# Performance work log

Measured on AMD Instinct MI355X. Metric: run time of the kernel, lower is better.

Reference implementation:

```python
import jax, jax.numpy as jnp
import numpy as np
from jax import lax

H = 256       # hidden_size (hard-coded via .view(256,1) in source)
V = 10000     # vocab
NOPS = 9      # ops: 0 sum, 1 count, 2 diff, 3 greater, 4 lesser, 5 and, 6 or, 7 assign, 8 reset
COLS = 64
ROWS = 200000
T = 4         # num_time_steps
QLEN = 40
NNUM = 5


def setup_inputs() -> dict:
    key = jax.random.key(0)
    ks = jax.random.split(key, 16)
    s = 0.02
    return {
        'input_question': jax.random.randint(ks[0], (QLEN,), 0, V),
        'question_numbers': jax.random.normal(ks[1], (NNUM,), jnp.float32),
        'left_word_indices': jax.random.randint(ks[2], (NNUM,), 0, QLEN),
        'table': jax.random.normal(ks[3], (ROWS, COLS), jnp.float32),
        # question RNN params
        'E': jax.random.normal(ks[4], (V, H), jnp.float32) * s,
        'Wx': jax.random.normal(ks[5], (H, H), jnp.float32) * s,
        'Wh': jax.random.normal(ks[6], (H, H), jnp.float32) * s,
        'b': jnp.zeros((H,), jnp.float32),
        # selector params
        'W_op': jax.random.normal(ks[7], (H, 2 * H), jnp.float32) * s,
        'op_emb': jax.random.normal(ks[8], (NOPS, H), jnp.float32) * s,
        'W_col': jax.random.normal(ks[9], (H, 2 * H), jnp.float32) * s,
        'col_emb': jax.random.normal(ks[10], (COLS, H), jnp.float32) * s,
        # pivot embeddings U(0)=lesser, U(1)=greater
        'U': jax.random.normal(ks[11], (2, H), jnp.float32) * s,
        # history RNN params
        'W_hc': jax.random.normal(ks[12], (H, 2 * H), jnp.float32) * s,
        'W_hh': jax.random.normal(ks[13], (H, H), jnp.float32) * s,
    }


def reference(input_question, question_numbers, left_word_indices, table,
              E, Wx, Wh, b, W_op, op_emb, W_col, col_emb, U, W_hc, W_hh):
    rows = table.shape[0]
    # ---- question RNN (simple tanh RNN over embedded words) ----
    x = E[input_question]                                  # [Q, H]
    def cell(h, xt):
        hn = jnp.tanh(xt @ Wx + h @ Wh + b)
        return hn, hn
    q, states = lax.scan(cell, jnp.zeros((H,), table.dtype), x)   # q: [H], states: [Q, H]
    Z = states[left_word_indices]                          # z_matrix [N, H]

    # ---- pivots (train mode: soft attention over question numbers) ----
    beta_l = jax.nn.softmax(Z @ U[0])                      # [N]
    beta_g = jax.nn.softmax(Z @ U[1])
    l_pivot = beta_l @ question_numbers                    # scalar
    g_pivot = beta_g @ question_numbers

    row_selects = [jnp.ones((rows,), table.dtype)]
    scalars = [jnp.zeros((), table.dtype)]
    h_hist = jnp.zeros((H,), table.dtype)
    lookup = jnp.zeros(table.shape, table.dtype)

    for t in range(T):
        qh = jnp.concatenate([q, h_hist])                  # [2H]
        a_op = jax.nn.softmax(op_emb @ jnp.tanh(W_op @ qh))    # [NOPS]
        a_col = jax.nn.softmax(col_emb @ jnp.tanh(W_col @ qh)) # [COLS]

        rs1 = row_selects[-1]
        rs2 = row_selects[max(0, len(row_selects) - 2)]
        s1 = scalars[-1]
        s3 = scalars[max(0, len(scalars) - 3)]

        col_val = table @ a_col                            # [R] column-weighted table values
        g_sel = (table > g_pivot).astype(table.dtype) @ a_col  # [R]
        l_sel = (table < l_pivot).astype(table.dtype) @ a_col

        row_select = (a_op[3] * g_sel + a_op[4] * l_sel
                      + a_op[5] * jnp.minimum(rs1, rs2)
                      + a_op[6] * jnp.maximum(rs1, rs2)
                      + a_op[8] * 1.0
                      + (a_op[0] + a_op[1] + a_op[2] + a_op[7]) * rs1)

        scalar = (a_op[0] * (rs1 @ col_val)
                  + a_op[1] * jnp.sum(rs1)
                  + a_op[2] * (s3 - s1))

        lookup = a_op[7] * row_select[:, None] * a_col[None, :]   # [R, C]

        c = jnp.concatenate([a_op @ op_emb, a_col @ col_emb])     # [2H]
        h_hist = jnp.tanh(W_hc @ c + W_hh @ h_hist)

        row_selects.append(row_select)
        scalars.append(scalar)

    return scalars[-1], lookup
```

## Files before the change

kernel.cpp:

```cpp
#include <hip/hip_runtime.h>
#include <math.h>

#define H 256
#define COLSN 64
#define ROWSN 200000
#define T_STEPS 4
#define QLEN 40
#define NNUM 5
#define NOPS 9

#define WS_UBUF   0
#define WS_XWB    0
#define WS_Q      10240
#define WS_AOP    10496
#define WS_ACOL   10560
#define WS_PIV    10816
#define WS_TICKET 10818
#define WS_PACC8  10824
#define WS_ARR    10832
#define WS_XWDONE 10836
#define WS_MDONE  10837
#define WS_QDONE  10838
#define WS_MOP    11104
#define WS_MCOL   13408

#define NTBL_TILES  1563
#define NTBL_BLOCKS 782
#define NW 12
#define NXW 10
#define NMB 72
#define NFUSED (NW + 1 + NXW + NMB)

template<int CTRL>
__device__ __forceinline__ float dpp_add(float x) {
    int xi = __float_as_int(x);
    int yi = __builtin_amdgcn_update_dpp(0, xi, CTRL, 0xF, 0xF, true);
    return x + __int_as_float(yi);
}
#define DPP_XOR1 0xB1
#define DPP_XOR2 0x4E
#define DPP_HMIR 0x141
#define DPP_MIR  0x140

__device__ __forceinline__ float reduce16(float v) {
    v = dpp_add<DPP_XOR1>(v);
    v = dpp_add<DPP_XOR2>(v);
    v = dpp_add<DPP_HMIR>(v);
    v = dpp_add<DPP_MIR>(v);
    return v;
}

__device__ __forceinline__ float fast_tanh(float x) {
    float cx = fminf(15.f, fmaxf(-15.f, x));
    float e = __expf(2.f * cx);
    return __fdividef(e - 1.f, e + 1.f);
}

__device__ __forceinline__ float dot4(float4 a, float4 b) {
    return a.x * b.x + a.y * b.y + a.z * b.z + a.w * b.w;
}

__device__ __forceinline__ float aread(float* p) { return atomicAdd(p, 0.f); }

__device__ __forceinline__ int sw(int i) { return i + ((i >> 4) << 2); }

__global__ void k_zero(float* __restrict__ ws) {
    int t = threadIdx.x;
    if (t < 22) ws[WS_TICKET + t] = 0.f;
}

__global__ __launch_bounds__(1024) void k_fused(
        const int* __restrict__ iq, const int* __restrict__ lwi,
        const float* __restrict__ qn, const float* __restrict__ E,
        const float* __restrict__ Wx, const float* __restrict__ b,
        const float* __restrict__ Wh, const float* __restrict__ U,
        const float* __restrict__ W_op, const float* __restrict__ W_col,
        const float* __restrict__ W_hh, const float* __restrict__ W_hc,
        const float* __restrict__ op_emb, const float* __restrict__ col_emb,
        float* __restrict__ ws) {
    __shared__ __attribute__((aligned(16))) float smem[36864];
    const int tid = threadIdx.x;
    const int blk = blockIdx.x;

    if (blk < NW) {
        float* wlds  = smem;
        float* mlds  = smem + 16448;
        float* hl    = smem + 35136;
        float* Pl    = smem + 35456;
        float* uop   = smem + 35520;
        float* ucol  = smem + 35840;
        float* vhh   = smem + 36160;
        float* lgs   = smem + 36416;
        float* aop_s = smem + 36496;
        float* acol_s= smem + 36512;
        const int wb = blk * 64;
        const int r  = tid >> 4;
        const int p  = tid & 15;
        const int pb = p * 20;

        for (int idx = tid; idx < 64 * 64; idx += 1024) {
            int rr = idx >> 6, j4 = idx & 63;
            int o = wb + rr;
            const float* src = (o < 256) ? &W_op[(long)o * 512 + 256]
                             : (o < 512) ? &W_col[(long)(o - 256) * 512 + 256]
                             : &W_hh[(long)(o - 512) * 256];
            float4 v = *(const float4*)&src[j4 * 4];
            float* d = &wlds[rr * 257 + j4 * 4];
            d[0] = v.x; d[1] = v.y; d[2] = v.z; d[3] = v.w;
        }
        if (tid == 0) while (aread(&ws[WS_MDONE]) < NMB - 0.5f) __builtin_amdgcn_s_sleep(8);
        __syncthreads();
        for (int idx = tid; idx < 73 * 256; idx += 1024)
            mlds[idx] = aread(&ws[WS_MOP + idx]);
        if (tid == 0) while (aread(&ws[WS_QDONE]) < 0.5f) __builtin_amdgcn_s_sleep(8);
        __syncthreads();
        if (tid < 256) hl[sw(tid)] = aread(&ws[WS_Q + tid]);
        __syncthreads();
        {
            int o = wb + r;
            float s = 0.f;
            if (o < 512) {
                const float* row = (o < 256) ? &W_op[(long)o * 512 + p * 16]
                                             : &W_col[(long)(o - 256) * 512 + p * 16];
                float4 r0 = *(const float4*)&row[0];
                float4 r1 = *(const float4*)&row[4];
                float4 r2 = *(const float4*)&row[8];
                float4 r3 = *(const float4*)&row[12];
                const float* qq = &hl[pb];
                s = dot4(r0, *(const float4*)&qq[0]) + dot4(r1, *(const float4*)&qq[4])
                  + dot4(r2, *(const float4*)&qq[8]) + dot4(r3, *(const float4*)&qq[12]);
            }
            s = reduce16(s);
            if (p == 0) Pl[r] = s;
        }
        __syncthreads();
        if (tid < 64) {
            int o = wb + tid;
            float val = (o < 512) ? fast_tanh(Pl[tid]) : 0.f;
            atomicExch(&ws[WS_UBUF + 0 * 768 + o], val);
        }
        __threadfence();
        __syncthreads();
        if (tid == 0) atomicAdd(&ws[WS_ARR + 0], 1.f);

        for (int t = 0; t < T_STEPS; ++t) {
            if (tid == 0) while (aread(&ws[WS_ARR + t]) < NW - 0.5f) __builtin_amdgcn_s_sleep(1);
            __syncthreads();
            if (tid < 256) {
                uop[sw(tid)]  = aread(&ws[WS_UBUF + t * 768 + tid]);
                ucol[sw(tid)] = aread(&ws[WS_UBUF + t * 768 + 256 + tid]);
                vhh[tid]      = aread(&ws[WS_UBUF + t * 768 + 512 + tid]);
            }
            __syncthreads();
            {
                const float* urow = &ucol[pb];
                float4 u0 = *(const float4*)&urow[0];
                float4 u1 = *(const float4*)&urow[4];
                float4 u2 = *(const float4*)&urow[8];
                float4 u3 = *(const float4*)&urow[12];
                const float* erow = &col_emb[r * 256 + p * 16];
                float4 e0 = *(const float4*)&erow[0];
                float4 e1 = *(const float4*)&erow[4];
                float4 e2 = *(const float4*)&erow[8];
                float4 e3 = *(const float4*)&erow[12];
                float s = dot4(e0, u0) + dot4(e1, u1) + dot4(e2, u2) + dot4(e3, u3);
                s = reduce16(s);
                if (p == 0) lgs[NOPS + r] = s;
                if (r < NOPS) {
                    const float* vrow = &uop[pb];
                    float4 v0 = *(const float4*)&vrow[0];
                    float4 v1 = *(const float4*)&vrow[4];
                    float4 v2 = *(const float4*)&vrow[8];
                    float4 v3 = *(const float4*)&vrow[12];
                    const float* orow = &op_emb[r * 256 + p * 16];
                    float4 f0 = *(const float4*)&orow[0];
                    float4 f1 = *(const float4*)&orow[4];
                    float4 f2 = *(const float4*)&orow[8];
                    float4 f3 = *(const float4*)&orow[12];
                    float so = dot4(f0, v0) + dot4(f1, v1) + dot4(f2, v2) + dot4(f3, v3);
                    so = reduce16(so);
                    if (p == 0) lgs[r] = so;
                }
            }
            __syncthreads();
            if (tid == 0) {
                float m = -1e30f;
                for (int k = 0; k < NOPS; ++k) m = fmaxf(m, lgs[k]);
                float e[NOPS], s = 0.f;
                for (int k = 0; k < NOPS; ++k) { e[k] = expf(lgs[k] - m); s += e[k]; }
                float inv = 1.f / s;
                for (int k = 0; k < NOPS; ++k) {
                    float a = e[k] * inv;
                    aop_s[k] = a;
                    if (blk == 0) ws[WS_AOP + t * 16 + k] = a;
                }
            }
            if (tid >= 64 && tid < 128) {
                int lane = tid - 64;
                float v = lgs[NOPS + lane];
                float m = v;
                for (int off = 1; off < 64; off <<= 1) m = fmaxf(m, __shfl_xor(m, off));
                float e = expf(v - m);
                float s = e;
                for (int off = 1; off < 64; off <<= 1) s += __shfl_xor(s, off);
                float a = __fdividef(e, s);
                acol_s[lane] = a;
                if (blk == 0) ws[WS_ACOL + t * COLSN + lane] = a;
            }
            __syncthreads();
            if (t < T_STEPS - 1) {
                if (tid < 256) {
                    float s = vhh[tid];
                    #pragma unroll
                    for (int k = 0; k < NOPS; ++k) s += aop_s[k] * mlds[k * 256 + tid];
                    #pragma unroll 8
                    for (int c = 0; c < COLSN; ++c) s += acol_s[c] * mlds[(NOPS + c) * 256 + tid];
                    hl[sw(tid)] = fast_tanh(s);
                }
                __syncthreads();
                {
                    int o = wb + r;
                    const float* wr = &wlds[r * 257 + p * 16];
                    float4 w0 = *(const float4*)&wr[0];
                    float4 w1 = *(const float4*)&wr[4];
                    float4 w2 = *(const float4*)&wr[8];
                    float4 w3 = *(const float4*)&wr[12];
                    const float* hh = &hl[pb];
                    float s = dot4(w0, *(const float4*)&hh[0]) + dot4(w1, *(const float4*)&hh[4])
                            + dot4(w2, *(const float4*)&hh[8]) + dot4(w3, *(const float4*)&hh[12]);
                    s = reduce16(s);
                    if (p == 0) {
                        float val = (o < 512) ? fast_tanh(Pl[r] + s) : s;
                        atomicExch(&ws[WS_UBUF + (t + 1) * 768 + o], val);
                    }
                }
                __threadfence();
                __syncthreads();
                if (tid == 0) atomicAdd(&ws[WS_ARR + t + 1], 1.f);
            }
        }
    } else if (blk == NW) {
        float* xwb  = smem;
        float* hbuf = smem + 10240;
        float* Z    = smem + 10816;
        float* lg   = smem + 12096;
        int g = tid >> 3;
        int p = tid & 7;

        float2 w2[32];
        #pragma unroll
        for (int jj = 0; jj < 32; ++jj)
            w2[jj] = *(const float2*)&Wh[(p * 32 + jj) * H + g * 2];

        if (tid == 0) while (aread(&ws[WS_XWDONE]) < NXW - 0.5f) __builtin_amdgcn_s_sleep(8);
        __syncthreads();
        for (int idx = tid; idx < QLEN * H; idx += 1024) xwb[idx] = aread(&ws[WS_XWB + idx]);
        if (tid < H) hbuf[0 * 288 + tid + ((tid >> 5) << 2)] = 0.f;
        __syncthreads();

        int lw0 = lwi[0], lw1 = lwi[1], lw2 = lwi[2], lw3 = lwi[3], lw4 = lwi[4];
        int cur = 0;
        for (int t = 0; t < QLEN; ++t) {
            const float4* hv = (const float4*)&hbuf[cur * 288 + p * 36];
            float a0 = 0.f, a1 = 0.f;
            #pragma unroll
            for (int q4 = 0; q4 < 8; ++q4) {
                float4 h4 = hv[q4];
                float2 wa = w2[q4 * 4 + 0];
                float2 wb2 = w2[q4 * 4 + 1];
                float2 wc = w2[q4 * 4 + 2];
                float2 wd = w2[q4 * 4 + 3];
                a0 += h4.x * wa.x; a1 += h4.x * wa.y;
                a0 += h4.y * wb2.x; a1 += h4.y * wb2.y;
                a0 += h4.z * wc.x; a1 += h4.z * wc.y;
                a0 += h4.w * wd.x; a1 += h4.w * wd.y;
            }
            a0 = dpp_add<DPP_XOR1>(a0); a0 = dpp_add<DPP_XOR2>(a0); a0 = dpp_add<DPP_HMIR>(a0);
            a1 = dpp_add<DPP_XOR1>(a1); a1 = dpp_add<DPP_XOR2>(a1); a1 = dpp_add<DPP_HMIR>(a1);
            if (p < 2) {
                float s = (p == 0) ? a0 : a1;
                int i = g * 2 + p;
                float hn = fast_tanh(xwb[t * H + i] + s);
                hbuf[(cur ^ 1) * 288 + i + ((i >> 5) << 2)] = hn;
                if (t == lw0) Z[0 * 256 + i] = hn;
                if (t == lw1) Z[1 * 256 + i] = hn;
                if (t == lw2) Z[2 * 256 + i] = hn;
                if (t == lw3) Z[3 * 256 + i] = hn;
                if (t == lw4) Z[4 * 256 + i] = hn;
            }
            __syncthreads();
            cur ^= 1;
        }
        if (tid < H) atomicExch(&ws[WS_Q + tid], hbuf[cur * 288 + tid + ((tid >> 5) << 2)]);

        int grp = tid >> 5;
        int lane = tid & 31;
        if (grp < 10) {
            int u = grp / 5, n = grp % 5;
            float s = 0.f;
            #pragma unroll
            for (int k = 0; k < 8; ++k) {
                int j = lane + k * 32;
                s += Z[n * 256 + j] * U[u * H + j];
            }
            s += __shfl_xor(s, 1);
            s += __shfl_xor(s, 2);
            s += __shfl_xor(s, 4);
            s += __shfl_xor(s, 8);
            s += __shfl_xor(s, 16);
            if (lane == 0) lg[grp] = s;
        }
        __syncthreads();
        if (tid < 2) {
            float m = -1e30f;
            for (int n = 0; n < 5; ++n) m = fmaxf(m, lg[tid * 5 + n]);
            float e[5], s = 0.f;
            for (int n = 0; n < 5; ++n) { e[n] = expf(lg[tid * 5 + n] - m); s += e[n]; }
            float piv = 0.f;
            for (int n = 0; n < 5; ++n) piv += (e[n] / s) * qn[n];
            ws[WS_PIV + (tid == 0 ? 1 : 0)] = piv;
        }
        __threadfence();
        __syncthreads();
        if (tid == 0) atomicAdd(&ws[WS_QDONE], 1.f);
    } else if (blk < NW + 1 + NXW) {
        int widx = (blk - NW - 1) * 4 + (tid >> 8);
        int i = tid & 255;
        int word = iq[widx];
        const float* erow = E + (long)word * H;
        float a0 = b[i], a1 = 0.f, a2 = 0.f, a3 = 0.f;
        #pragma unroll 8
        for (int j = 0; j < H; j += 4) {
            a0 += erow[j + 0] * Wx[(j + 0) * H + i];
            a1 += erow[j + 1] * Wx[(j + 1) * H + i];
            a2 += erow[j + 2] * Wx[(j + 2) * H + i];
            a3 += erow[j + 3] * Wx[(j + 3) * H + i];
        }
        atomicExch(&ws[WS_XWB + widx * H + i], (a0 + a1) + (a2 + a3));
        __threadfence();
        __syncthreads();
        if (tid == 0) atomicAdd(&ws[WS_XWDONE], 1.f);
    } else {
        float* tile = smem;
        int mb = blk - NW - 1 - NXW;
        int bi = mb / 9;
        int kg = mb % 9;
        int ibase = bi * 32;
        int coff = (kg == 0) ? 0 : H;
        for (int idx = tid; idx < 32 * 64; idx += 1024) {
            int rr = idx >> 6, c4 = idx & 63;
            float4 v = *(const float4*)&W_hc[(long)(ibase + rr) * 512 + coff + c4 * 4];
            float* d = &tile[rr * 268 + c4 * 4];
            d[0] = v.x; d[1] = v.y; d[2] = v.z; d[3] = v.w;
        }
        __syncthreads();
        int io = tid >> 5;
        int l32 = tid & 31;
        int nk = (kg == 0) ? NOPS : 8;
        for (int kk = 0; kk < nk; ++kk) {
            const float* emb;
            int dst;
            if (kg == 0) { emb = op_emb + kk * H; dst = WS_MOP + kk * H; }
            else { int c = (kg - 1) * 8 + kk; emb = col_emb + c * H; dst = WS_MCOL + c * H; }
            float s = 0.f;
            #pragma unroll
            for (int q8 = 0; q8 < 8; ++q8) {
                int q = (q8 + l32) & 7;
                s += tile[io * 268 + l32 * 8 + q] * emb[l32 * 8 + q];
            }
            s += __shfl_xor(s, 1);
            s += __shfl_xor(s, 2);
            s += __shfl_xor(s, 4);
            s += __shfl_xor(s, 8);
            s += __shfl_xor(s, 16);
            if (l32 == 0) atomicExch(&ws[dst + ibase + io], s);
        }
        __threadfence();
        __syncthreads();
        if (tid == 0) atomicAdd(&ws[WS_MDONE], 1.f);
    }
}

__global__ __launch_bounds__(512) void k_table(const float* __restrict__ table,
                                               float* __restrict__ ws,
                                               float* __restrict__ out) {
    __shared__ __attribute__((aligned(16))) float4 acT4[4][17];
    __shared__ float aop_l[64];
    __shared__ float rs3s[8][16];
    __shared__ float bred[8][8];
    __shared__ int lastblk;
    const int tid = threadIdx.x;
    const int wid = tid >> 6;
    const int lane = tid & 63;
    const int r16 = lane & 15;
    const int q = lane >> 4;

    if (tid < 64) {
        aop_l[tid] = ws[WS_AOP + tid];
        acT4[tid >> 4][tid & 15] = make_float4(
            ws[WS_ACOL + 0 * COLSN + tid], ws[WS_ACOL + 1 * COLSN + tid],
            ws[WS_ACOL + 2 * COLSN + tid], ws[WS_ACOL + 3 * COLSN + tid]);
    }
    __syncthreads();
    const float gp = ws[WS_PIV + 0];
    const float lp = ws[WS_PIV + 1];
    const float ac3 = acT4[q][r16].w;

    float dacc[4] = {0,0,0,0}, cacc[4] = {0,0,0,0};

    for (int tile = blockIdx.x; tile < NTBL_TILES; tile += NTBL_BLOCKS) {
        long wrow = (long)tile * 128 + wid * 16;
        bool active = wrow < ROWSN;

        float cv[4] = {0,0,0,0}, gs[4] = {0,0,0,0}, ls[4] = {0,0,0,0};
        if (active) {
            const float* src = table + (wrow + r16) * COLSN + q * 16;
            float4 x0 = *(const float4*)&src[0];
            float4 x1 = *(const float4*)&src[4];
            float4 x2 = *(const float4*)&src[8];
            float4 x3 = *(const float4*)&src[12];
            float xs[16] = {x0.x,x0.y,x0.z,x0.w, x1.x,x1.y,x1.z,x1.w,
                            x2.x,x2.y,x2.z,x2.w, x3.x,x3.y,x3.z,x3.w};
            #pragma unroll
            for (int jj = 0; jj < 16; ++jj) {
                float x = xs[jj];
                float4 a4 = acT4[q][jj];
                float gt = (x > gp) ? 1.f : 0.f;
                float lt = (x < lp) ? 1.f : 0.f;
                cv[0] += x * a4.x;  cv[1] += x * a4.y;  cv[2] += x * a4.z;  cv[3] += x * a4.w;
                gs[0] += gt * a4.x; gs[1] += gt * a4.y; gs[2] += gt * a4.z; gs[3] += gt * a4.w;
                ls[0] += lt * a4.x; ls[1] += lt * a4.y; ls[2] += lt * a4.z; ls[3] += lt * a4.w;
            }
        }
        #pragma unroll
        for (int k = 0; k < 4; ++k) {
            cv[k] += __shfl_xor(cv[k], 16); cv[k] += __shfl_xor(cv[k], 32);
            gs[k] += __shfl_xor(gs[k], 16); gs[k] += __shfl_xor(gs[k], 32);
            ls[k] += __shfl_xor(ls[k], 16); ls[k] += __shfl_xor(ls[k], 32);
        }

        float prev1 = 1.f, prev2 = 1.f;
        #pragma unroll
        for (int t = 0; t < 4; ++t) {
            if (active) { dacc[t] += prev1 * cv[t]; cacc[t] += prev1; }
            float cg = aop_l[t*16+3], cl = aop_l[t*16+4], cmn = aop_l[t*16+5];
            float cmx = aop_l[t*16+6], co = aop_l[t*16+8];
            float cid = aop_l[t*16+0] + aop_l[t*16+1] + aop_l[t*16+2] + aop_l[t*16+7];
            float rsn = cg * gs[t] + cl * ls[t] + cmn * fminf(prev1, prev2)
                      + cmx * fmaxf(prev1, prev2) + co + cid * prev1;
            prev2 = prev1; prev1 = rsn;
        }
        if (q == 0 && active) rs3s[wid][r16] = prev1 * aop_l[3*16+7];

        if (active) {
            float* dst = out + 1 + wrow * COLSN;
            #pragma unroll 4
            for (int s = 0; s < 16; ++s)
                dst[(long)s * COLSN + lane] = rs3s[wid][s] * ac3;
        }
    }

    float vals[8];
    #pragma unroll
    for (int t = 0; t < 4; ++t) { vals[t] = dacc[t]; vals[4 + t] = cacc[t]; }
    #pragma unroll
    for (int k = 0; k < 8; ++k) vals[k] = reduce16(vals[k]);
    if (lane == 0) {
        #pragma unroll
        for (int k = 0; k < 8; ++k) bred[wid][k] = vals[k];
    }
    __syncthreads();
    if (tid < 8) {
        float s = 0.f;
        #pragma unroll
        for (int w = 0; w < 8; ++w) s += bred[w][tid];
        atomicAdd(&ws[WS_PACC8 + tid], s);
    }
    __syncthreads();

    if (tid == 0) {
        float old = atomicAdd(&ws[WS_TICKET], 1.0f);
        lastblk = ((int)(old + 0.5f) == NTBL_BLOCKS - 1) ? 1 : 0;
    }
    __syncthreads();
    if (lastblk) {
        if (tid < 8) bred[0][tid] = atomicAdd(&ws[WS_PACC8 + tid], 0.f);
        __syncthreads();
        if (tid == 0) {
            float d0 = bred[0][0], d1 = bred[0][1], d2 = bred[0][2], d3 = bred[0][3];
            float c0 = bred[0][4], c1 = bred[0][5], c2 = bred[0][6], c3 = bred[0][7];
            float s0 = aop_l[0]*d0  + aop_l[1]*c0;
            float s1 = aop_l[16]*d1 + aop_l[17]*c1 + aop_l[18]*(0.f - s0);
            float s2 = aop_l[32]*d2 + aop_l[33]*c2 + aop_l[34]*(0.f - s1);
            float s3 = aop_l[48]*d3 + aop_l[49]*c3 + aop_l[50]*(s0 - s2);
            out[0] = s3;
        }
    }
}

extern "C" void kernel_launch(void* const* d_in, const int* in_sizes, int n_in,
                              void* d_out, int out_size, void* d_ws, size_t ws_size,
                              hipStream_t stream) {
    const int*   iq      = (const int*)  d_in[0];
    const float* qn      = (const float*)d_in[1];
    const int*   lwi     = (const int*)  d_in[2];
    const float* table   = (const float*)d_in[3];
    const float* E       = (const float*)d_in[4];
    const float* Wx      = (const float*)d_in[5];
    const float* Wh      = (const float*)d_in[6];
    const float* b       = (const float*)d_in[7];
    const float* W_op    = (const float*)d_in[8];
    const float* op_emb  = (const float*)d_in[9];
    const float* W_col   = (const float*)d_in[10];
    const float* col_emb = (const float*)d_in[11];
    const float* U       = (const float*)d_in[12];
    const float* W_hc    = (const float*)d_in[13];
    const float* W_hh    = (const float*)d_in[14];
    float* out = (float*)d_out;
    float* ws  = (float*)d_ws;

    hipLaunchKernelGGL(k_zero, dim3(1), dim3(64), 0, stream, ws);
    hipLaunchKernelGGL(k_fused, dim3(NFUSED), dim3(1024), 0, stream,
                       iq, lwi, qn, E, Wx, b, Wh, U, W_op, W_col, W_hh,
                       W_hc, op_emb, col_emb, ws);
    hipLaunchKernelGGL(k_table, dim3(NTBL_BLOCKS), dim3(512), 0, stream,
                       table, ws, out);
}
```

Baseline: 143.8 us.

## Split fused persistent kernel into separate pre, RNN, and selector launches

The word-projection and question-RNN roles move out of the single persistent fused kernel into their own kernels, k_pre and k_rnn, launched in stream order ahead of the selector kernel. Stream ordering replaces the XWDONE and QDONE spin-wait flags and the atomic reads and writes used to pass data between blocks, and the zeroing kernel is folded into k_pre. The cost is extra launch gaps and lost overlap: the selector blocks' weight loading and the W_hc/embedding products can no longer run alongside the serial RNN. The spin-wait sleep interval is also shortened.

```diff
diff --git a/kernel.cpp b/kernel.cpp
--- a/kernel.cpp
+++ b/kernel.cpp
@@ -18,18 +18,15 @@
 #define WS_TICKET 10818
 #define WS_PACC8  10824
 #define WS_ARR    10832
-#define WS_XWDONE 10836
 #define WS_MDONE  10837
-#define WS_QDONE  10838
 #define WS_MOP    11104
 #define WS_MCOL   13408
 
 #define NTBL_TILES  1563
 #define NTBL_BLOCKS 782
 #define NW 12
-#define NXW 10
 #define NMB 72
-#define NFUSED (NW + 1 + NXW + NMB)
+#define NSELF (NW + NMB)
 
 template<int CTRL>
 __device__ __forceinline__ float dpp_add(float x) {
@@ -64,16 +61,116 @@
 
 __device__ __forceinline__ int sw(int i) { return i + ((i >> 4) << 2); }
 
-__global__ void k_zero(float* __restrict__ ws) {
-    int t = threadIdx.x;
-    if (t < 22) ws[WS_TICKET + t] = 0.f;
-}
-
-__global__ __launch_bounds__(1024) void k_fused(
-        const int* __restrict__ iq, const int* __restrict__ lwi,
-        const float* __restrict__ qn, const float* __restrict__ E,
-        const float* __restrict__ Wx, const float* __restrict__ b,
-        const float* __restrict__ Wh, const float* __restrict__ U,
+__global__ __launch_bounds__(1024) void k_pre(const int* __restrict__ iq,
+        const float* __restrict__ E, const float* __restrict__ Wx,
+        const float* __restrict__ b, float* __restrict__ ws) {
+    int tid = threadIdx.x;
+    if (blockIdx.x == 0 && tid < 22) ws[WS_TICKET + tid] = 0.f;
+    int widx = blockIdx.x * 4 + (tid >> 8);
+    int i = tid & 255;
+    int word = iq[widx];
+    const float* erow = E + (long)word * H;
+    float a0 = b[i], a1 = 0.f, a2 = 0.f, a3 = 0.f;
+    #pragma unroll 8
+    for (int j = 0; j < H; j += 4) {
+        a0 += erow[j + 0] * Wx[(j + 0) * H + i];
+        a1 += erow[j + 1] * Wx[(j + 1) * H + i];
+        a2 += erow[j + 2] * Wx[(j + 2) * H + i];
+        a3 += erow[j + 3] * Wx[(j + 3) * H + i];
+    }
+    ws[WS_XWB + widx * H + i] = (a0 + a1) + (a2 + a3);
+}
+
+__global__ __launch_bounds__(1024) void k_rnn(const float* __restrict__ Wh,
+                      const int* __restrict__ lwi,
+                      const float* __restrict__ U, const float* __restrict__ qn,
+                      float* __restrict__ ws) {
+    __shared__ __attribute__((aligned(16))) float hbuf[2][288];
+    __shared__ __attribute__((aligned(16))) float xwb[QLEN][H];
+    __shared__ float Z[NNUM][H];
+    __shared__ float lg[10];
+    int tid = threadIdx.x;
+    int g = tid >> 3;
+    int p = tid & 7;
+
+    float2 w2[32];
+    #pragma unroll
+    for (int jj = 0; jj < 32; ++jj)
+        w2[jj] = *(const float2*)&Wh[(p * 32 + jj) * H + g * 2];
+
+    {
+        const float4* src = (const float4*)&ws[WS_XWB];
+        float4* dst = (float4*)&xwb[0][0];
+        for (int idx = tid; idx < QLEN * H / 4; idx += 1024) dst[idx] = src[idx];
+    }
+    if (tid < H) hbuf[0][tid + ((tid >> 5) << 2)] = 0.f;
+    __syncthreads();
+
+    int lw0 = lwi[0], lw1 = lwi[1], lw2 = lwi[2], lw3 = lwi[3], lw4 = lwi[4];
+    int cur = 0;
+    for (int t = 0; t < QLEN; ++t) {
+        const float4* hv = (const float4*)&hbuf[cur][p * 36];
+        float a0 = 0.f, a1 = 0.f;
+        #pragma unroll
+        for (int q4 = 0; q4 < 8; ++q4) {
+            float4 h4 = hv[q4];
+            float2 wa = w2[q4 * 4 + 0];
+            float2 wb = w2[q4 * 4 + 1];
+            float2 wc = w2[q4 * 4 + 2];
+            float2 wd = w2[q4 * 4 + 3];
+            a0 += h4.x * wa.x; a1 += h4.x * wa.y;
+            a0 += h4.y * wb.x; a1 += h4.y * wb.y;
+            a0 += h4.z * wc.x; a1 += h4.z * wc.y;
+            a0 += h4.w * wd.x; a1 += h4.w * wd.y;
+        }
+        a0 = dpp_add<DPP_XOR1>(a0); a0 = dpp_add<DPP_XOR2>(a0); a0 = dpp_add<DPP_HMIR>(a0);
+        a1 = dpp_add<DPP_XOR1>(a1); a1 = dpp_add<DPP_XOR2>(a1); a1 = dpp_add<DPP_HMIR>(a1);
+        if (p < 2) {
+            float s = (p == 0) ? a0 : a1;
+            int i = g * 2 + p;
+            float hn = fast_tanh(xwb[t][i] + s);
+            hbuf[cur ^ 1][i + ((i >> 5) << 2)] = hn;
+            if (t == lw0) Z[0][i] = hn;
+            if (t == lw1) Z[1][i] = hn;
+            if (t == lw2) Z[2][i] = hn;
+            if (t == lw3) Z[3][i] = hn;
+            if (t == lw4) Z[4][i] = hn;
+        }
+        __syncthreads();
+        cur ^= 1;
+    }
+    if (tid < H) ws[WS_Q + tid] = hbuf[cur][tid + ((tid >> 5) << 2)];
+
+    int grp = tid >> 5;
+    int lane = tid & 31;
+    if (grp < 10) {
+        int u = grp / 5, n = grp % 5;
+        float s = 0.f;
+        #pragma unroll
+        for (int k = 0; k < 8; ++k) {
+            int j = lane + k * 32;
+            s += Z[n][j] * U[u * H + j];
+        }
+        s += __shfl_xor(s, 1);
+        s += __shfl_xor(s, 2);
+        s += __shfl_xor(s, 4);
+        s += __shfl_xor(s, 8);
+        s += __shfl_xor(s, 16);
+        if (lane == 0) lg[grp] = s;
+    }
+    __syncthreads();
+    if (tid < 2) {
+        float m = -1e30f;
+        for (int n = 0; n < 5; ++n) m = fmaxf(m, lg[tid * 5 + n]);
+        float e[5], s = 0.f;
+        for (int n = 0; n < 5; ++n) { e[n] = expf(lg[tid * 5 + n] - m); s += e[n]; }
+        float piv = 0.f;
+        for (int n = 0; n < 5; ++n) piv += (e[n] / s) * qn[n];
+        ws[WS_PIV + (tid == 0 ? 1 : 0)] = piv;
+    }
+}
+
+__global__ __launch_bounds__(1024) void k_selF(
         const float* __restrict__ W_op, const float* __restrict__ W_col,
         const float* __restrict__ W_hh, const float* __restrict__ W_hc,
         const float* __restrict__ op_emb, const float* __restrict__ col_emb,
@@ -108,13 +205,11 @@
             float* d = &wlds[rr * 257 + j4 * 4];
             d[0] = v.x; d[1] = v.y; d[2] = v.z; d[3] = v.w;
         }
-        if (tid == 0) while (aread(&ws[WS_MDONE]) < NMB - 0.5f) __builtin_amdgcn_s_sleep(8);
+        if (tid < 256) hl[sw(tid)] = ws[WS_Q + tid];
+        if (tid == 0) while (aread(&ws[WS_MDONE]) < NMB - 0.5f) __builtin_amdgcn_s_sleep(1);
         __syncthreads();
         for (int idx = tid; idx < 73 * 256; idx += 1024)
             mlds[idx] = aread(&ws[WS_MOP + idx]);
-        if (tid == 0) while (aread(&ws[WS_QDONE]) < 0.5f) __builtin_amdgcn_s_sleep(8);
-        __syncthreads();
-        if (tid < 256) hl[sw(tid)] = aread(&ws[WS_Q + tid]);
         __syncthreads();
         {
             int o = wb + r;
@@ -239,110 +334,9 @@
                 if (tid == 0) atomicAdd(&ws[WS_ARR + t + 1], 1.f);
             }
         }
-    } else if (blk == NW) {
-        float* xwb  = smem;
-        float* hbuf = smem + 10240;
-        float* Z    = smem + 10816;
-        float* lg   = smem + 12096;
-        int g = tid >> 3;
-        int p = tid & 7;
-
-        float2 w2[32];
-        #pragma unroll
-        for (int jj = 0; jj < 32; ++jj)
-            w2[jj] = *(const float2*)&Wh[(p * 32 + jj) * H + g * 2];
-
-        if (tid == 0) while (aread(&ws[WS_XWDONE]) < NXW - 0.5f) __builtin_amdgcn_s_sleep(8);
-        __syncthreads();
-        for (int idx = tid; idx < QLEN * H; idx += 1024) xwb[idx] = aread(&ws[WS_XWB + idx]);
-        if (tid < H) hbuf[0 * 288 + tid + ((tid >> 5) << 2)] = 0.f;
-        __syncthreads();
-
-        int lw0 = lwi[0], lw1 = lwi[1], lw2 = lwi[2], lw3 = lwi[3], lw4 = lwi[4];
-        int cur = 0;
-        for (int t = 0; t < QLEN; ++t) {
-            const float4* hv = (const float4*)&hbuf[cur * 288 + p * 36];
-            float a0 = 0.f, a1 = 0.f;
-            #pragma unroll
-            for (int q4 = 0; q4 < 8; ++q4) {
-                float4 h4 = hv[q4];
-                float2 wa = w2[q4 * 4 + 0];
-                float2 wb2 = w2[q4 * 4 + 1];
-                float2 wc = w2[q4 * 4 + 2];
-                float2 wd = w2[q4 * 4 + 3];
-                a0 += h4.x * wa.x; a1 += h4.x * wa.y;
-                a0 += h4.y * wb2.x; a1 += h4.y * wb2.y;
-                a0 += h4.z * wc.x; a1 += h4.z * wc.y;
-                a0 += h4.w * wd.x; a1 += h4.w * wd.y;
-            }
-            a0 = dpp_add<DPP_XOR1>(a0); a0 = dpp_add<DPP_XOR2>(a0); a0 = dpp_add<DPP_HMIR>(a0);
-            a1 = dpp_add<DPP_XOR1>(a1); a1 = dpp_add<DPP_XOR2>(a1); a1 = dpp_add<DPP_HMIR>(a1);
-            if (p < 2) {
-                float s = (p == 0) ? a0 : a1;
-                int i = g * 2 + p;
-                float hn = fast_tanh(xwb[t * H + i] + s);
-                hbuf[(cur ^ 1) * 288 + i + ((i >> 5) << 2)] = hn;
-                if (t == lw0) Z[0 * 256 + i] = hn;
-                if (t == lw1) Z[1 * 256 + i] = hn;
-                if (t == lw2) Z[2 * 256 + i] = hn;
-                if (t == lw3) Z[3 * 256 + i] = hn;
-                if (t == lw4) Z[4 * 256 + i] = hn;
-            }
-            __syncthreads();
-            cur ^= 1;
-        }
-        if (tid < H) atomicExch(&ws[WS_Q + tid], hbuf[cur * 288 + tid + ((tid >> 5) << 2)]);
-
-        int grp = tid >> 5;
-        int lane = tid & 31;
-        if (grp < 10) {
-            int u = grp / 5, n = grp % 5;
-            float s = 0.f;
-            #pragma unroll
-            for (int k = 0; k < 8; ++k) {
-                int j = lane + k * 32;
-                s += Z[n * 256 + j] * U[u * H + j];
-            }
-            s += __shfl_xor(s, 1);
-            s += __shfl_xor(s, 2);
-            s += __shfl_xor(s, 4);
-            s += __shfl_xor(s, 8);
-            s += __shfl_xor(s, 16);
-            if (lane == 0) lg[grp] = s;
-        }
-        __syncthreads();
-        if (tid < 2) {
-            float m = -1e30f;
-            for (int n = 0; n < 5; ++n) m = fmaxf(m, lg[tid * 5 + n]);
-            float e[5], s = 0.f;
-            for (int n = 0; n < 5; ++n) { e[n] = expf(lg[tid * 5 + n] - m); s += e[n]; }
-            float piv = 0.f;
-            for (int n = 0; n < 5; ++n) piv += (e[n] / s) * qn[n];
-            ws[WS_PIV + (tid == 0 ? 1 : 0)] = piv;
-        }
-        __threadfence();
-        __syncthreads();
-        if (tid == 0) atomicAdd(&ws[WS_QDONE], 1.f);
-    } else if (blk < NW + 1 + NXW) {
-        int widx = (blk - NW - 1) * 4 + (tid >> 8);
-        int i = tid & 255;
-        int word = iq[widx];
-        const float* erow = E + (long)word * H;
-        float a0 = b[i], a1 = 0.f, a2 = 0.f, a3 = 0.f;
-        #pragma unroll 8
-        for (int j = 0; j < H; j += 4) {
-            a0 += erow[j + 0] * Wx[(j + 0) * H + i];
-            a1 += erow[j + 1] * Wx[(j + 1) * H + i];
-            a2 += erow[j + 2] * Wx[(j + 2) * H + i];
-            a3 += erow[j + 3] * Wx[(j + 3) * H + i];
-        }
-        atomicExch(&ws[WS_XWB + widx * H + i], (a0 + a1) + (a2 + a3));
-        __threadfence();
-        __syncthreads();
-        if (tid == 0) atomicAdd(&ws[WS_XWDONE], 1.f);
     } else {
         float* tile = smem;
-        int mb = blk - NW - 1 - NXW;
+        int mb = blk - NW;
         int bi = mb / 9;
         int kg = mb % 9;
         int ibase = bi * 32;
@@ -519,10 +513,10 @@
     float* out = (float*)d_out;
     float* ws  = (float*)d_ws;
 
-    hipLaunchKernelGGL(k_zero, dim3(1), dim3(64), 0, stream, ws);
-    hipLaunchKernelGGL(k_fused, dim3(NFUSED), dim3(1024), 0, stream,
-                       iq, lwi, qn, E, Wx, b, Wh, U, W_op, W_col, W_hh,
-                       W_hc, op_emb, col_emb, ws);
+    hipLaunchKernelGGL(k_pre,  dim3(10), dim3(1024), 0, stream, iq, E, Wx, b, ws);
+    hipLaunchKernelGGL(k_rnn,  dim3(1), dim3(1024), 0, stream, Wh, lwi, U, qn, ws);
+    hipLaunchKernelGGL(k_selF, dim3(NSELF), dim3(1024), 0, stream,
+                       W_op, W_col, W_hh, W_hc, op_emb, col_emb, ws);
     hipLaunchKernelGGL(k_table, dim3(NTBL_BLOCKS), dim3(512), 0, stream,
                        table, ws, out);
 }
```

After: 170.0 us. 18.2% more time.
